# Kernel tuning notes

Measured on AMD Instinct MI355X. Metric: run time of the kernel, lower is better.

## Reference

```python
import jax, jax.numpy as jnp
import numpy as np

B, K, E = 8192, 16, 64          # subgraphs, nodes/subgraph, edges/subgraph
FIN, FOUT = 300, 64
ALPHA, BETA = 1.0, 0.6
EPS = 1e-12


def _l2n(x):
    # F.normalize(x, p=2, dim=-1)
    return x / jnp.maximum(jnp.linalg.norm(x, axis=-1, keepdims=True), EPS)


def _flat(idx):
    # local node ids -> global ids in the batched graph (offset b*K)
    return (idx + (jnp.arange(B, dtype=idx.dtype) * K)[:, None]).ravel()


def _spmm(src_f, dst_f, w, x):
    # h[dst] += w * x[src]  over all B*E edges; x: [B,K,F]
    F = x.shape[-1]
    xf = x.reshape(B * K, F)
    msg = xf[src_f] * w.ravel()[:, None]
    return jnp.zeros((B * K, F), x.dtype).at[dst_f].add(msg).reshape(B, K, F)


def _deg_inv_sqrt(idx_f):
    d = jnp.zeros((B * K,), jnp.float32).at[idx_f].add(1.0)
    return jnp.clip(d, 1.0) ** -0.5


def _enc(feat, src, dst, w, W, b):
    # OneLayerGCNWithGlobalAdg: zero anchor feat, GraphConv(norm='none', edge_weight), ReLU
    anchor_out = jax.nn.relu(feat[:, 0, :] @ W + b)          # [B,FOUT]
    fz = feat.at[:, 0, :].set(0.0)
    x = fz @ W                                               # [B,K,FOUT]
    h = jax.nn.relu(_spmm(_flat(src), _flat(dst), w, x) + b)
    pool = h.mean(axis=1)                                    # mean over all K nodes
    return _l2n(h), _l2n(pool), _l2n(anchor_out)


def _dec(h, src, dst, w, W, b):
    # OneLayerGCN: GraphConv(norm='both', edge_weight), ReLU
    sf, df = _flat(src), _flat(dst)
    nsrc = _deg_inv_sqrt(sf).reshape(B, K, 1)   # out-degree^-1/2
    ndst = _deg_inv_sqrt(df).reshape(B, K, 1)   # in-degree^-1/2
    x = (h * nsrc) @ W                          # project first (FOUT < FIN)
    hd = jax.nn.relu(_spmm(sf, df, w, x) * ndst + b)
    pool = hd[:, :-1, :].mean(axis=1)           # mean over nodes [:-1]
    anchor = hd[:, 0, :]
    return _l2n(hd), _l2n(pool), _l2n(anchor)


def setup_inputs() -> dict:
    key = jax.random.key(0)
    ks = jax.random.split(key, 16)
    g_enc = float(np.sqrt(6.0 / (FIN + FOUT)))
    g_dec = float(np.sqrt(6.0 / (FOUT + FIN)))
    g_bil = float(np.sqrt(6.0 / (FOUT + FOUT)))
    inp = {
        'feat_p1': jax.random.normal(ks[0], (B, K, FIN), jnp.float32),
        'feat_p2': jax.random.normal(ks[1], (B, K, FIN), jnp.float32),
        'feat_n':  jax.random.normal(ks[2], (B, K, FIN), jnp.float32),
        'w_p1': jax.random.uniform(ks[3], (B, E), jnp.float32),
        'w_p2': jax.random.uniform(ks[4], (B, E), jnp.float32),
        'w_n':  jax.random.uniform(ks[5], (B, E), jnp.float32),
        'W_enc': jax.random.uniform(ks[6], (FIN, FOUT), jnp.float32, -g_enc, g_enc),
        'b_enc': jnp.zeros((FOUT,), jnp.float32),
        'W_dec': jax.random.uniform(ks[7], (FOUT, FIN), jnp.float32, -g_dec, g_dec),
        'b_dec': jnp.zeros((FIN,), jnp.float32),
        'W_bil': jax.random.uniform(ks[8], (FOUT, FOUT), jnp.float32, -g_bil, g_bil),
        'b_bil': jnp.zeros((1,), jnp.float32),
        'src_p1': jax.random.randint(ks[9], (B, E), 0, K, jnp.int32),
        'dst_p1': jax.random.randint(ks[10], (B, E), 0, K, jnp.int32),
        'src_p2': jax.random.randint(ks[11], (B, E), 0, K, jnp.int32),
        'dst_p2': jax.random.randint(ks[12], (B, E), 0, K, jnp.int32),
        'src_n':  jax.random.randint(ks[13], (B, E), 0, K, jnp.int32),
        'dst_n':  jax.random.randint(ks[14], (B, E), 0, K, jnp.int32),
    }
    return inp


def reference(feat_p1, feat_p2, feat_n, w_p1, w_p2, w_n,
              W_enc, b_enc, W_dec, b_dec, W_bil, b_bil,
              src_p1, dst_p1, src_p2, dst_p2, src_n, dst_n):
    ori1 = feat_p1[:, 0, :]
    ori2 = feat_p2[:, 0, :]

    h1, pool1, a1 = _enc(feat_p1, src_p1, dst_p1, w_p1, W_enc, b_enc)
    h2, pool2, a2 = _enc(feat_p2, src_p2, dst_p2, w_p2, W_enc, b_enc)
    _, pooln, _ = _enc(feat_n, src_n, dst_n, w_n, W_enc, b_enc)

    def disc(r, a):  # nn.Bilinear(FOUT, FOUT, 1)
        return jnp.einsum('bj,jk,bk->b', r, W_bil, a)[:, None] + b_bil

    ps1 = jax.nn.sigmoid(disc(pool1, a1))
    ps2 = jax.nn.sigmoid(disc(pool2, a2))
    ns1 = jax.nn.sigmoid(disc(pooln, a1))
    ns2 = jax.nn.sigmoid(disc(pooln, a2))

    _, _, da1 = _dec(h1, src_p1, dst_p1, w_p1, W_dec, b_dec)
    _, _, da2 = _dec(h2, src_p2, dst_p2, w_p2, W_dec, b_dec)

    m1 = jnp.mean(jnp.log(ps1) + jnp.log(1.0 - ns1))
    m2 = jnp.mean(jnp.log(ps2) + jnp.log(1.0 - ns2))
    L_con = -((m1 / 2 + m2 / 2) / 2)
    L_gen = (jnp.mean(jnp.square(da1 - ori1)) + jnp.mean(jnp.square(da2 - ori2))) / 2
    L = ALPHA * L_con + BETA * L_gen

    attributes_num = jnp.sqrt(jnp.float32(FIN))
    contr = (ns1 - ps1 + 1.0) / 2 + (ns2 - ps2 + 1.0) / 2          # [B,1]
    gen = (jnp.linalg.norm(da1 - ori1) / attributes_num / 2
           + jnp.linalg.norm(da2 - ori2) / attributes_num / 2)      # scalar
    single_predict_scores = ALPHA * contr + BETA * gen
    return L, single_predict_scores
```

## Files before the change

kernel.cpp:

```cpp
#include <hip/hip_runtime.h>

#define BB 8192
#define KK 16
#define EE 64
#define FINN 300

typedef __attribute__((ext_vector_type(8))) short short8;
typedef __attribute__((ext_vector_type(4))) float f32x4;

__device__ __forceinline__ unsigned packbf(float a, float b) {
  unsigned ua = __float_as_uint(a), ub = __float_as_uint(b);
  ua = (ua + 0x7fffu + ((ua >> 16) & 1u)) >> 16;
  ub = (ub + 0x7fffu + ((ub >> 16) & 1u)) >> 16;
  return ua | (ub << 16);
}
__device__ __forceinline__ float redC(float v) {
  v += __shfl_xor(v, 1); v += __shfl_xor(v, 2);
  v += __shfl_xor(v, 4); v += __shfl_xor(v, 8);
  return v;
}
__device__ __forceinline__ float redQ(float v) {
  v += __shfl_xor(v, 16); v += __shfl_xor(v, 32);
  return v;
}
__device__ __forceinline__ float waveSum(float v) {
#pragma unroll
  for (int off = 32; off; off >>= 1) v += __shfl_xor(v, off);
  return v;
}
__device__ __forceinline__ float logsig(float z) {
  return fminf(z, 0.f) - log1pf(expf(-fabsf(z)));
}

__global__ void prep_kernel(const float* __restrict__ Wenc, uint4* __restrict__ wB) {
  const int id = blockIdx.x * 256 + threadIdx.x;
  if (id >= 2560) return;
  const int lane = id & 63;
  const int step = (id >> 6) % 10;
  const int nt = id / 640;
  const int n = nt * 16 + (lane & 15);
  const int kb = step * 32 + (lane >> 4) * 8;
  float f[8];
#pragma unroll
  for (int j2 = 0; j2 < 8; ++j2) {
    const int k = kb + j2;
    f[j2] = (k < FINN) ? Wenc[k * 64 + n] : 0.f;
  }
  uint4 o;
  o.x = packbf(f[0], f[1]); o.y = packbf(f[2], f[3]);
  o.z = packbf(f[4], f[5]); o.w = packbf(f[6], f[7]);
  wB[id] = o;
}

__global__ __launch_bounds__(256, 3) void enc_kernel(
    const float* __restrict__ feat, const float* __restrict__ wedg,
    const int* __restrict__ src, const int* __restrict__ dst,
    const uint4* __restrict__ wB, const float* __restrict__ benc,
    float* __restrict__ pool_out, float* __restrict__ a_out,
    float* __restrict__ g_out, float* __restrict__ nd0_out)
{
  __shared__ char smem[41984];
  unsigned* featU = (unsigned*)smem;
  char* xBc = smem;
  float* AdjL = (float*)(smem + 16384);
  char* AdjBc = smem + 20480;
  float* coefL = (float*)(smem + 24576);
  float* xAnch = (float*)(smem + 24832);

  const int tid = threadIdx.x, lane = tid & 63, wv = tid >> 6;
  const int q = lane >> 4, c = lane & 15;
  const int b0 = blockIdx.x * 4;

  uint4 bfr[10];
  {
    const uint4* p = wB + (wv * 10) * 64 + lane;
#pragma unroll
    for (int s = 0; s < 10; ++s) bfr[s] = p[s * 64];
  }
  {
    const float4* gf = (const float4*)(feat + (size_t)b0 * (KK * FINN));
    for (int it = tid; it < 4800; it += 256) {
      const float4 v = gf[it];
      const int row = it / 75, c4 = it - row * 75;
      unsigned* p = featU + row * 164 + c4 * 2;
      p[0] = packbf(v.x, v.y);
      p[1] = packbf(v.z, v.w);
    }
    for (int it = tid; it < 896; it += 256)
      featU[(it / 14) * 164 + 150 + (it % 14)] = 0;
  }
  __syncthreads();

  f32x4 acc[4];
#pragma unroll
  for (int m = 0; m < 4; ++m) acc[m] = (f32x4){0.f, 0.f, 0.f, 0.f};
#pragma unroll
  for (int s = 0; s < 10; ++s) {
    const short8 b8 = *(const short8*)&bfr[s];
#pragma unroll
    for (int m = 0; m < 4; ++m) {
      const short8 a8 = *(const short8*)(smem + (m * 16 + c) * 656 + s * 64 + q * 16);
      acc[m] = __builtin_amdgcn_mfma_f32_16x16x32_bf16(a8, b8, acc[m], 0, 0, 0);
    }
  }
  __syncthreads();

#pragma unroll
  for (int m = 0; m < 4; ++m) {
    unsigned* dp = (unsigned*)(xBc + ((m * 4 + wv) * 64 + (q >> 1) * 16 + c) * 16 + (q & 1) * 8);
    dp[0] = packbf(acc[m][0], acc[m][1]);
    dp[1] = packbf(acc[m][2], acc[m][3]);
    if (q == 0) xAnch[m * 64 + wv * 16 + c] = acc[m][0];
  }
  {
    const uint4 z = {0, 0, 0, 0};
    for (int i = tid; i < 512; i += 256)
      ((uint4*)xBc)[(i >> 5) * 64 + 32 + (i & 31)] = z;
    for (int i = tid; i < 512; i += 256)
      ((uint4*)(smem + 16384))[i] = z;
  }
  __syncthreads();

  const int g = wv;
  const int bu = b0 + wv;
  const int se = src[bu * EE + lane];
  const int de = dst[bu * EE + lane];
  const float we = wedg[bu * EE + lane];

  float dinv_reg = 0.f;
#pragma unroll
  for (int k = 0; k < KK; ++k) {
    const int cnt = __popcll(__ballot(se == k));
    if (lane == k) dinv_reg = rsqrtf(fmaxf((float)cnt, 1.f));
  }
  if (nd0_out) {
    const int cd0 = __popcll(__ballot(de == 0));
    if (lane == 0) nd0_out[bu] = rsqrtf(fmaxf((float)cd0, 1.f));
  }
  atomicAdd(&AdjL[g * 256 + de * 16 + se], we);
  __threadfence_block();
  {
    const f32x4 v = *(const f32x4*)(AdjL + g * 256 + lane * 4);
    const float v0 = ((lane & 3) == 0) ? 0.f : v[0];
    unsigned* w = (unsigned*)(AdjBc + g * 1024 + (lane >> 2) * 64 + (lane & 3) * 8);
    w[0] = packbf(v0, v[1]);
    w[1] = packbf(v[2], v[3]);
  }
  if (g_out && lane < KK)
    coefL[g * 16 + lane] = AdjL[g * 256 + lane] * dinv_reg;
  __threadfence_block();

  const short8 aAdj = *(const short8*)(AdjBc + g * 1024 + c * 64 + q * 16);
  float bj[4], h[4][4];
#pragma unroll
  for (int nt = 0; nt < 4; ++nt) bj[nt] = benc[nt * 16 + c];
#pragma unroll
  for (int nt = 0; nt < 4; ++nt) {
    const short8 xb = *(const short8*)(xBc + ((g * 4 + nt) * 64 + lane) * 16);
    f32x4 cc = (f32x4){0.f, 0.f, 0.f, 0.f};
    cc = __builtin_amdgcn_mfma_f32_16x16x32_bf16(aAdj, xb, cc, 0, 0, 0);
#pragma unroll
    for (int r = 0; r < 4; ++r) h[nt][r] = fmaxf(cc[r] + bj[nt], 0.f);
  }

  float pl[4];
#pragma unroll
  for (int nt = 0; nt < 4; ++nt)
    pl[nt] = redQ(h[nt][0] + h[nt][1] + h[nt][2] + h[nt][3]);
  float pn2 = redC(pl[0] * pl[0] + pl[1] * pl[1] + pl[2] * pl[2] + pl[3] * pl[3]);
  const float pinv = 1.f / fmaxf(sqrtf(pn2), 1e-12f);
  if (q == 0)
#pragma unroll
    for (int nt = 0; nt < 4; ++nt)
      pool_out[(size_t)bu * 64 + nt * 16 + c] = pl[nt] * pinv;

  if (g_out) {
    float rnv[4];
#pragma unroll
    for (int r = 0; r < 4; ++r) {
      float s2 = redC(h[0][r] * h[0][r] + h[1][r] * h[1][r] +
                      h[2][r] * h[2][r] + h[3][r] * h[3][r]);
      rnv[r] = 1.f / fmaxf(sqrtf(s2), 1e-12f);
    }
    float gp[4] = {0.f, 0.f, 0.f, 0.f};
#pragma unroll
    for (int r = 0; r < 4; ++r) {
      const float cf = coefL[g * 16 + q * 4 + r] * rnv[r];
#pragma unroll
      for (int nt = 0; nt < 4; ++nt) gp[nt] = fmaf(cf, h[nt][r], gp[nt]);
    }
#pragma unroll
    for (int nt = 0; nt < 4; ++nt) gp[nt] = redQ(gp[nt]);
    if (q == 1)
#pragma unroll
      for (int nt = 0; nt < 4; ++nt)
        g_out[(size_t)bu * 64 + nt * 16 + c] = gp[nt];
  }
  if (a_out) {
    float av[4], an2 = 0.f;
#pragma unroll
    for (int nt = 0; nt < 4; ++nt) {
      av[nt] = fmaxf(xAnch[g * 64 + nt * 16 + c] + bj[nt], 0.f);
      an2 += av[nt] * av[nt];
    }
    an2 = redC(an2);
    const float ainv = 1.f / fmaxf(sqrtf(an2), 1e-12f);
    if (q == 2)
#pragma unroll
      for (int nt = 0; nt < 4; ++nt)
        a_out[(size_t)bu * 64 + nt * 16 + c] = av[nt] * ainv;
  }
}

__global__ __launch_bounds__(256) void dec_kernel(
    const float* __restrict__ g_buf, const float* __restrict__ nd0_buf,
    const float* __restrict__ Wdec, const float* __restrict__ bdec,
    const float* __restrict__ feat, float* __restrict__ dArr)
{
  __shared__ float red[8];
  __shared__ float invn_s;
  const int t = threadIdx.x, b = blockIdx.x;
  const float gv = g_buf[(size_t)b * 64 + (t & 63)];
  const float nd0 = nd0_buf[b];
  const int f0 = t, f1 = t + 256;
  const bool has1 = (f1 < FINN);
  float y0 = 0.f, y1 = 0.f;
  for (int jj = 0; jj < 64; ++jj) {
    const float gj = __shfl(gv, jj);
    y0 = fmaf(gj, Wdec[jj * FINN + f0], y0);
    if (has1) y1 = fmaf(gj, Wdec[jj * FINN + f1], y1);
  }
  const float a0 = fmaxf(y0 * nd0 + bdec[f0], 0.f);
  const float a1 = has1 ? fmaxf(y1 * nd0 + bdec[f1], 0.f) : 0.f;
  float ss = waveSum(a0 * a0 + a1 * a1);
  if ((t & 63) == 0) red[t >> 6] = ss;
  __syncthreads();
  if (t == 0) invn_s = 1.f / fmaxf(sqrtf(red[0] + red[1] + red[2] + red[3]), 1e-12f);
  __syncthreads();
  const float inv = invn_s;
  const float* __restrict__ ori = feat + (size_t)b * KK * FINN;
  const float d0 = a0 * inv - ori[f0];
  const float d1 = has1 ? (a1 * inv - ori[f1]) : 0.f;
  float sd = waveSum(d0 * d0 + d1 * d1);
  if ((t & 63) == 0) red[4 + (t >> 6)] = sd;
  __syncthreads();
  if (t == 0) dArr[b] = red[4] + red[5] + red[6] + red[7];
}

__global__ __launch_bounds__(256) void bil_kernel(
    const float* __restrict__ pool1, const float* __restrict__ pool2,
    const float* __restrict__ pooln, const float* __restrict__ a1b,
    const float* __restrict__ a2b, const float* __restrict__ Wbil,
    const float* __restrict__ bbil, float* __restrict__ contr,
    float* __restrict__ tArr1, float* __restrict__ tArr2)
{
  const int tid = threadIdx.x, wv = tid >> 6, j = tid & 63;
  const int bu = blockIdx.x * 4 + wv;
  const float p1 = pool1[(size_t)bu * 64 + j];
  const float p2 = pool2[(size_t)bu * 64 + j];
  const float pn = pooln[(size_t)bu * 64 + j];
  const float A1 = a1b[(size_t)bu * 64 + j];
  const float A2 = a2b[(size_t)bu * 64 + j];
  float v1 = 0.f, v2 = 0.f, vn = 0.f;
  for (int jj = 0; jj < 64; ++jj) {
    const float wr = Wbil[jj * 64 + j];
    v1 = fmaf(__shfl(p1, jj), wr, v1);
    v2 = fmaf(__shfl(p2, jj), wr, v2);
    vn = fmaf(__shfl(pn, jj), wr, vn);
  }
  const float d11 = waveSum(v1 * A1);
  const float d22 = waveSum(v2 * A2);
  const float dn1 = waveSum(vn * A1);
  const float dn2 = waveSum(vn * A2);
  if (j == 0) {
    const float bb = bbil[0];
    const float z11 = d11 + bb, z22 = d22 + bb, zn1 = dn1 + bb, zn2 = dn2 + bb;
    const float ps1 = 1.f / (1.f + expf(-z11));
    const float ps2 = 1.f / (1.f + expf(-z22));
    const float ns1 = 1.f / (1.f + expf(-zn1));
    const float ns2 = 1.f / (1.f + expf(-zn2));
    contr[bu] = (ns1 - ps1 + 1.f) * 0.5f + (ns2 - ps2 + 1.f) * 0.5f;
    tArr1[bu] = logsig(z11) + logsig(-zn1);
    tArr2[bu] = logsig(z22) + logsig(-zn2);
  }
}

__global__ __launch_bounds__(256) void reduce_kernel(const float* __restrict__ parts,
                                                     double* __restrict__ accs)
{
  __shared__ double sred[4];
  const int t = threadIdx.x, lane = t & 63, wv = t >> 6;
  const float* __restrict__ p = parts + (size_t)blockIdx.x * BB;
  double s = 0.0;
  for (int i = t; i < BB; i += 256) s += (double)p[i];
#pragma unroll
  for (int off = 32; off; off >>= 1) s += __shfl_xor(s, off);
  if (lane == 0) sred[wv] = s;
  __syncthreads();
  if (t == 0) accs[blockIdx.x] = sred[0] + sred[1] + sred[2] + sred[3];
}

__global__ void fin_kernel(const double* __restrict__ acc, float* __restrict__ genw,
                           float* __restrict__ out)
{
  const double T1 = acc[0], T2 = acc[1], S1d = acc[2], S2d = acc[3];
  const double m1 = S1d / (double)BB, m2 = S2d / (double)BB;
  const double Lcon = -(m1 + m2) * 0.25;
  const double Lgen = (T1 + T2) / (2.0 * (double)BB * (double)FINN);
  out[0] = (float)(Lcon + 0.6 * Lgen);
  genw[0] = (float)((sqrt(T1) + sqrt(T2)) / (2.0 * sqrt((double)FINN)));
}

__global__ void score_kernel(const float* __restrict__ contr, const float* __restrict__ genw,
                             float* __restrict__ out)
{
  const int i = blockIdx.x * blockDim.x + threadIdx.x;
  if (i < BB) out[1 + i] = fmaf(0.6f, genw[0], contr[i]);
}

extern "C" void kernel_launch(void* const* d_in, const int* in_sizes, int n_in,
                              void* d_out, int out_size, void* d_ws, size_t ws_size,
                              hipStream_t stream)
{
  const float* feat_p1 = (const float*)d_in[0];
  const float* feat_p2 = (const float*)d_in[1];
  const float* feat_n  = (const float*)d_in[2];
  const float* w_p1 = (const float*)d_in[3];
  const float* w_p2 = (const float*)d_in[4];
  const float* w_n  = (const float*)d_in[5];
  const float* W_enc = (const float*)d_in[6];
  const float* b_enc = (const float*)d_in[7];
  const float* W_dec = (const float*)d_in[8];
  const float* b_dec = (const float*)d_in[9];
  const float* W_bil = (const float*)d_in[10];
  const float* b_bil = (const float*)d_in[11];
  const int* src_p1 = (const int*)d_in[12];
  const int* dst_p1 = (const int*)d_in[13];
  const int* src_p2 = (const int*)d_in[14];
  const int* dst_p2 = (const int*)d_in[15];
  const int* src_n  = (const int*)d_in[16];
  const int* dst_n  = (const int*)d_in[17];
  float* out = (float*)d_out;

  double* accs = (double*)d_ws;
  float* genw = (float*)((char*)d_ws + 32);
  uint4* wsB = (uint4*)((char*)d_ws + 1024);
  float* fws = (float*)((char*)d_ws + 49152);
  float* pool1 = fws;
  float* pool2 = pool1 + (size_t)BB * 64;
  float* pooln = pool2 + (size_t)BB * 64;
  float* a1 = pooln + (size_t)BB * 64;
  float* a2 = a1 + (size_t)BB * 64;
  float* g1 = a2 + (size_t)BB * 64;
  float* g2 = g1 + (size_t)BB * 64;
  float* nd01 = g2 + (size_t)BB * 64;
  float* nd02 = nd01 + BB;
  float* contr = nd02 + BB;
  float* parts = contr + BB;
  float* dArr1 = parts;
  float* dArr2 = parts + BB;
  float* tArr1 = parts + 2 * BB;
  float* tArr2 = parts + 3 * BB;

  hipLaunchKernelGGL(prep_kernel, dim3(10), dim3(256), 0, stream, W_enc, wsB);
  hipLaunchKernelGGL(enc_kernel, dim3(BB / 4), dim3(256), 0, stream,
                     feat_n, w_n, src_n, dst_n, wsB, b_enc, pooln,
                     (float*)nullptr, (float*)nullptr, (float*)nullptr);
  hipLaunchKernelGGL(enc_kernel, dim3(BB / 4), dim3(256), 0, stream,
                     feat_p1, w_p1, src_p1, dst_p1, wsB, b_enc, pool1, a1, g1, nd01);
  hipLaunchKernelGGL(enc_kernel, dim3(BB / 4), dim3(256), 0, stream,
                     feat_p2, w_p2, src_p2, dst_p2, wsB, b_enc, pool2, a2, g2, nd02);
  hipLaunchKernelGGL(dec_kernel, dim3(BB), dim3(256), 0, stream,
                     g1, nd01, W_dec, b_dec, feat_p1, dArr1);
  hipLaunchKernelGGL(dec_kernel, dim3(BB), dim3(256), 0, stream,
                     g2, nd02, W_dec, b_dec, feat_p2, dArr2);
  hipLaunchKernelGGL(bil_kernel, dim3(BB / 4), dim3(256), 0, stream,
                     pool1, pool2, pooln, a1, a2, W_bil, b_bil, contr, tArr1, tArr2);
  hipLaunchKernelGGL(reduce_kernel, dim3(4), dim3(256), 0, stream, parts, accs);
  hipLaunchKernelGGL(fin_kernel, dim3(1), dim3(1), 0, stream, accs, genw, out);
  hipLaunchKernelGGL(score_kernel, dim3((BB + 255) / 256), dim3(256), 0, stream,
                     contr, genw, out);
}
```

Baseline: 655.9 us.

## Merge encoder launches, swizzle feature LDS, fuse decoders and final reductions

Runs the three encoder passes in one grid by decoding the input set from the block index. Replaces the padded LDS row stride with an XOR swizzle, which shrinks shared memory and lets launch bounds ask for 4 blocks per CU. Fuses the two decoder launches so each Wdec load serves both positive graphs, and merges the reduce and finalize kernels into a single 1024-thread block. The aim is fewer launches, better occupancy, fewer LDS bank conflicts and less redundant weight traffic, at the cost of more register pressure in the decoder and a single-block final reduction.

```diff
diff --git a/kernel.cpp b/kernel.cpp
--- a/kernel.cpp
+++ b/kernel.cpp
@@ -24,6 +24,11 @@
   return v;
 }
 __device__ __forceinline__ float waveSum(float v) {
+#pragma unroll
+  for (int off = 32; off; off >>= 1) v += __shfl_xor(v, off);
+  return v;
+}
+__device__ __forceinline__ double waveSumD(double v) {
 #pragma unroll
   for (int off = 32; off; off >>= 1) v += __shfl_xor(v, off);
   return v;
@@ -52,14 +57,18 @@
   wB[id] = o;
 }
 
-__global__ __launch_bounds__(256, 3) void enc_kernel(
-    const float* __restrict__ feat, const float* __restrict__ wedg,
-    const int* __restrict__ src, const int* __restrict__ dst,
+__global__ __launch_bounds__(256, 4) void enc_kernel(
+    const float* __restrict__ fpn, const float* __restrict__ fp1, const float* __restrict__ fp2,
+    const float* __restrict__ wn, const float* __restrict__ w1, const float* __restrict__ w2,
+    const int* __restrict__ sn, const int* __restrict__ s1, const int* __restrict__ s2,
+    const int* __restrict__ dn, const int* __restrict__ d1, const int* __restrict__ d2,
     const uint4* __restrict__ wB, const float* __restrict__ benc,
-    float* __restrict__ pool_out, float* __restrict__ a_out,
-    float* __restrict__ g_out, float* __restrict__ nd0_out)
-{
-  __shared__ char smem[41984];
+    float* __restrict__ pooln, float* __restrict__ pool1, float* __restrict__ pool2,
+    float* __restrict__ a1o, float* __restrict__ a2o,
+    float* __restrict__ g1o, float* __restrict__ g2o,
+    float* __restrict__ nd1o, float* __restrict__ nd2o)
+{
+  __shared__ char smem[40960];
   unsigned* featU = (unsigned*)smem;
   char* xBc = smem;
   float* AdjL = (float*)(smem + 16384);
@@ -69,7 +78,22 @@
 
   const int tid = threadIdx.x, lane = tid & 63, wv = tid >> 6;
   const int q = lane >> 4, c = lane & 15;
-  const int b0 = blockIdx.x * 4;
+  const int kf = blockIdx.x >> 11;
+  const int bg = blockIdx.x & 2047;
+  const int b0 = bg * 4;
+
+  const float* feat; const float* wedg; const int* src; const int* dst;
+  float* pool_out; float* a_out; float* g_out; float* nd0_out;
+  if (kf == 0) {
+    feat = fpn; wedg = wn; src = sn; dst = dn;
+    pool_out = pooln; a_out = nullptr; g_out = nullptr; nd0_out = nullptr;
+  } else if (kf == 1) {
+    feat = fp1; wedg = w1; src = s1; dst = d1;
+    pool_out = pool1; a_out = a1o; g_out = g1o; nd0_out = nd1o;
+  } else {
+    feat = fp2; wedg = w2; src = s2; dst = d2;
+    pool_out = pool2; a_out = a2o; g_out = g2o; nd0_out = nd2o;
+  }
 
   uint4 bfr[10];
   {
@@ -82,24 +106,28 @@
     for (int it = tid; it < 4800; it += 256) {
       const float4 v = gf[it];
       const int row = it / 75, c4 = it - row * 75;
-      unsigned* p = featU + row * 164 + c4 * 2;
-      p[0] = packbf(v.x, v.y);
-      p[1] = packbf(v.z, v.w);
-    }
-    for (int it = tid; it < 896; it += 256)
-      featU[(it / 14) * 164 + 150 + (it % 14)] = 0;
+      uint2 o;
+      o.x = packbf(v.x, v.y);
+      o.y = packbf(v.z, v.w);
+      *(uint2*)&featU[row * 160 + ((c4 * 2) ^ ((row & 7) << 2))] = o;
+    }
+    for (int it = tid; it < 640; it += 256) {
+      const int row = it / 10, dlog = 150 + (it - row * 10);
+      featU[row * 160 + (dlog ^ ((row & 7) << 2))] = 0;
+    }
   }
   __syncthreads();
 
   f32x4 acc[4];
 #pragma unroll
   for (int m = 0; m < 4; ++m) acc[m] = (f32x4){0.f, 0.f, 0.f, 0.f};
+  const int xr = (c & 7) << 4;
 #pragma unroll
   for (int s = 0; s < 10; ++s) {
     const short8 b8 = *(const short8*)&bfr[s];
 #pragma unroll
     for (int m = 0; m < 4; ++m) {
-      const short8 a8 = *(const short8*)(smem + (m * 16 + c) * 656 + s * 64 + q * 16);
+      const short8 a8 = *(const short8*)(smem + (m * 16 + c) * 640 + ((s * 64 + q * 16) ^ xr));
       acc[m] = __builtin_amdgcn_mfma_f32_16x16x32_bf16(a8, b8, acc[m], 0, 0, 0);
     }
   }
@@ -213,38 +241,62 @@
 }
 
 __global__ __launch_bounds__(256) void dec_kernel(
-    const float* __restrict__ g_buf, const float* __restrict__ nd0_buf,
+    const float* __restrict__ g1b, const float* __restrict__ g2b,
+    const float* __restrict__ nd1b, const float* __restrict__ nd2b,
     const float* __restrict__ Wdec, const float* __restrict__ bdec,
-    const float* __restrict__ feat, float* __restrict__ dArr)
-{
-  __shared__ float red[8];
-  __shared__ float invn_s;
+    const float* __restrict__ feat1, const float* __restrict__ feat2,
+    float* __restrict__ dArr1, float* __restrict__ dArr2)
+{
+  __shared__ float red[16];
+  __shared__ float invA_s, invB_s;
   const int t = threadIdx.x, b = blockIdx.x;
-  const float gv = g_buf[(size_t)b * 64 + (t & 63)];
-  const float nd0 = nd0_buf[b];
+  const float gva = g1b[(size_t)b * 64 + (t & 63)];
+  const float gvb = g2b[(size_t)b * 64 + (t & 63)];
+  const float nda = nd1b[b], ndb = nd2b[b];
   const int f0 = t, f1 = t + 256;
   const bool has1 = (f1 < FINN);
-  float y0 = 0.f, y1 = 0.f;
+  float ya0 = 0.f, ya1 = 0.f, yb0 = 0.f, yb1 = 0.f;
   for (int jj = 0; jj < 64; ++jj) {
-    const float gj = __shfl(gv, jj);
-    y0 = fmaf(gj, Wdec[jj * FINN + f0], y0);
-    if (has1) y1 = fmaf(gj, Wdec[jj * FINN + f1], y1);
-  }
-  const float a0 = fmaxf(y0 * nd0 + bdec[f0], 0.f);
-  const float a1 = has1 ? fmaxf(y1 * nd0 + bdec[f1], 0.f) : 0.f;
-  float ss = waveSum(a0 * a0 + a1 * a1);
-  if ((t & 63) == 0) red[t >> 6] = ss;
-  __syncthreads();
-  if (t == 0) invn_s = 1.f / fmaxf(sqrtf(red[0] + red[1] + red[2] + red[3]), 1e-12f);
-  __syncthreads();
-  const float inv = invn_s;
-  const float* __restrict__ ori = feat + (size_t)b * KK * FINN;
-  const float d0 = a0 * inv - ori[f0];
-  const float d1 = has1 ? (a1 * inv - ori[f1]) : 0.f;
-  float sd = waveSum(d0 * d0 + d1 * d1);
-  if ((t & 63) == 0) red[4 + (t >> 6)] = sd;
-  __syncthreads();
-  if (t == 0) dArr[b] = red[4] + red[5] + red[6] + red[7];
+    const float w0 = Wdec[jj * FINN + f0];
+    const float ga = __shfl(gva, jj), gb = __shfl(gvb, jj);
+    ya0 = fmaf(ga, w0, ya0);
+    yb0 = fmaf(gb, w0, yb0);
+    if (has1) {
+      const float w1 = Wdec[jj * FINN + f1];
+      ya1 = fmaf(ga, w1, ya1);
+      yb1 = fmaf(gb, w1, yb1);
+    }
+  }
+  const float bd0 = bdec[f0];
+  const float bd1 = has1 ? bdec[f1] : 0.f;
+  const float aa0 = fmaxf(ya0 * nda + bd0, 0.f);
+  const float aa1 = has1 ? fmaxf(ya1 * nda + bd1, 0.f) : 0.f;
+  const float ab0 = fmaxf(yb0 * ndb + bd0, 0.f);
+  const float ab1 = has1 ? fmaxf(yb1 * ndb + bd1, 0.f) : 0.f;
+  float sA = waveSum(aa0 * aa0 + aa1 * aa1);
+  float sB = waveSum(ab0 * ab0 + ab1 * ab1);
+  if ((t & 63) == 0) { red[t >> 6] = sA; red[8 + (t >> 6)] = sB; }
+  __syncthreads();
+  if (t == 0) {
+    invA_s = 1.f / fmaxf(sqrtf(red[0] + red[1] + red[2] + red[3]), 1e-12f);
+    invB_s = 1.f / fmaxf(sqrtf(red[8] + red[9] + red[10] + red[11]), 1e-12f);
+  }
+  __syncthreads();
+  const float invA = invA_s, invB = invB_s;
+  const float* __restrict__ ori1 = feat1 + (size_t)b * KK * FINN;
+  const float* __restrict__ ori2 = feat2 + (size_t)b * KK * FINN;
+  const float dA0 = aa0 * invA - ori1[f0];
+  const float dA1 = has1 ? (aa1 * invA - ori1[f1]) : 0.f;
+  const float dB0 = ab0 * invB - ori2[f0];
+  const float dB1 = has1 ? (ab1 * invB - ori2[f1]) : 0.f;
+  float sdA = waveSum(dA0 * dA0 + dA1 * dA1);
+  float sdB = waveSum(dB0 * dB0 + dB1 * dB1);
+  if ((t & 63) == 0) { red[t >> 6] = sdA; red[8 + (t >> 6)] = sdB; }
+  __syncthreads();
+  if (t == 0) {
+    dArr1[b] = red[0] + red[1] + red[2] + red[3];
+    dArr2[b] = red[8] + red[9] + red[10] + red[11];
+  }
 }
 
 __global__ __launch_bounds__(256) void bil_kernel(
@@ -285,30 +337,30 @@
   }
 }
 
-__global__ __launch_bounds__(256) void reduce_kernel(const float* __restrict__ parts,
-                                                     double* __restrict__ accs)
-{
-  __shared__ double sred[4];
+__global__ __launch_bounds__(1024) void redfin_kernel(const float* __restrict__ parts,
+                                                      float* __restrict__ genw,
+                                                      float* __restrict__ out)
+{
+  __shared__ double sred[16];
   const int t = threadIdx.x, lane = t & 63, wv = t >> 6;
-  const float* __restrict__ p = parts + (size_t)blockIdx.x * BB;
+  const int seg = t >> 8;
+  const float* __restrict__ p = parts + (size_t)seg * BB;
   double s = 0.0;
-  for (int i = t; i < BB; i += 256) s += (double)p[i];
-#pragma unroll
-  for (int off = 32; off; off >>= 1) s += __shfl_xor(s, off);
+  for (int i = (t & 255); i < BB; i += 256) s += (double)p[i];
+  s = waveSumD(s);
   if (lane == 0) sred[wv] = s;
   __syncthreads();
-  if (t == 0) accs[blockIdx.x] = sred[0] + sred[1] + sred[2] + sred[3];
-}
-
-__global__ void fin_kernel(const double* __restrict__ acc, float* __restrict__ genw,
-                           float* __restrict__ out)
-{
-  const double T1 = acc[0], T2 = acc[1], S1d = acc[2], S2d = acc[3];
-  const double m1 = S1d / (double)BB, m2 = S2d / (double)BB;
-  const double Lcon = -(m1 + m2) * 0.25;
-  const double Lgen = (T1 + T2) / (2.0 * (double)BB * (double)FINN);
-  out[0] = (float)(Lcon + 0.6 * Lgen);
-  genw[0] = (float)((sqrt(T1) + sqrt(T2)) / (2.0 * sqrt((double)FINN)));
+  if (t == 0) {
+    const double T1 = sred[0] + sred[1] + sred[2] + sred[3];
+    const double T2 = sred[4] + sred[5] + sred[6] + sred[7];
+    const double S1d = sred[8] + sred[9] + sred[10] + sred[11];
+    const double S2d = sred[12] + sred[13] + sred[14] + sred[15];
+    const double m1 = S1d / (double)BB, m2 = S2d / (double)BB;
+    const double Lcon = -(m1 + m2) * 0.25;
+    const double Lgen = (T1 + T2) / (2.0 * (double)BB * (double)FINN);
+    out[0] = (float)(Lcon + 0.6 * Lgen);
+    genw[0] = (float)((sqrt(T1) + sqrt(T2)) / (2.0 * sqrt((double)FINN)));
+  }
 }
 
 __global__ void score_kernel(const float* __restrict__ contr, const float* __restrict__ genw,
@@ -342,7 +394,6 @@
   const int* dst_n  = (const int*)d_in[17];
   float* out = (float*)d_out;
 
-  double* accs = (double*)d_ws;
   float* genw = (float*)((char*)d_ws + 32);
   uint4* wsB = (uint4*)((char*)d_ws + 1024);
   float* fws = (float*)((char*)d_ws + 49152);
@@ -363,21 +414,19 @@
   float* tArr2 = parts + 3 * BB;
 
   hipLaunchKernelGGL(prep_kernel, dim3(10), dim3(256), 0, stream, W_enc, wsB);
-  hipLaunchKernelGGL(enc_kernel, dim3(BB / 4), dim3(256), 0, stream,
-                     feat_n, w_n, src_n, dst_n, wsB, b_enc, pooln,
-                     (float*)nullptr, (float*)nullptr, (float*)nullptr);
-  hipLaunchKernelGGL(enc_kernel, dim3(BB / 4), dim3(256), 0, stream,
-                     feat_p1, w_p1, src_p1, dst_p1, wsB, b_enc, pool1, a1, g1, nd01);
-  hipLaunchKernelGGL(enc_kernel, dim3(BB / 4), dim3(256), 0, stream,
-                     feat_p2, w_p2, src_p2, dst_p2, wsB, b_enc, pool2, a2, g2, nd02);
+  hipLaunchKernelGGL(enc_kernel, dim3(3 * BB / 4), dim3(256), 0, stream,
+                     feat_n, feat_p1, feat_p2,
+                     w_n, w_p1, w_p2,
+                     src_n, src_p1, src_p2,
+                     dst_n, dst_p1, dst_p2,
+                     wsB, b_enc,
+                     pooln, pool1, pool2,
+                     a1, a2, g1, g2, nd01, nd02);
   hipLaunchKernelGGL(dec_kernel, dim3(BB), dim3(256), 0, stream,
-                     g1, nd01, W_dec, b_dec, feat_p1, dArr1);
-  hipLaunchKernelGGL(dec_kernel, dim3(BB), dim3(256), 0, stream,
-                     g2, nd02, W_dec, b_dec, feat_p2, dArr2);
+                     g1, g2, nd01, nd02, W_dec, b_dec, feat_p1, feat_p2, dArr1, dArr2);
   hipLaunchKernelGGL(bil_kernel, dim3(BB / 4), dim3(256), 0, stream,
                      pool1, pool2, pooln, a1, a2, W_bil, b_bil, contr, tArr1, tArr2);
-  hipLaunchKernelGGL(reduce_kernel, dim3(4), dim3(256), 0, stream, parts, accs);
-  hipLaunchKernelGGL(fin_kernel, dim3(1), dim3(1), 0, stream, accs, genw, out);
+  hipLaunchKernelGGL(redfin_kernel, dim3(1), dim3(1024), 0, stream, parts, genw, out);
   hipLaunchKernelGGL(score_kernel, dim3((BB + 255) / 256), dim3(256), 0, stream,
                      contr, genw, out);
 }
```

Result: faster. 584.7 us (-10.9%).
